# Optimization experiments

Measured on AMD Instinct MI355X. Metric: run time of the kernel, lower is better.

## Reference

```python
import jax, jax.numpy as jnp
import numpy as np

N_HEAD = 16
HEAD_DIM = 128

def rotate_half(x):
    x1, x2 = jnp.split(x, 2, axis=-1)
    return jnp.concatenate((-x2, x1), axis=-1)

def setup_inputs() -> dict:
    key = jax.random.key(0)
    ks = jax.random.split(key, 5)
    B, T, C = 2, 2048, 2048
    x = jax.random.normal(ks[0], (B, T, C), dtype=jnp.float32)
    # rotary tables as used by the module: cos/sin of shape [T, head_dim]
    pos = jnp.arange(T, dtype=jnp.float32)[:, None]
    inv_freq = 1.0 / (10000.0 ** (jnp.arange(0, HEAD_DIM, 2, dtype=jnp.float32) / HEAD_DIM))
    freqs = pos * inv_freq[None, :]            # [T, head_dim/2]
    emb = jnp.concatenate([freqs, freqs], -1)  # [T, head_dim]
    cos = jnp.cos(emb)
    sin = jnp.sin(emb)
    W_qkv = jax.random.normal(ks[1], (C, 3 * C), dtype=jnp.float32) * (C ** -0.5)
    W_proj = jax.random.normal(ks[2], (C, C), dtype=jnp.float32) * (C ** -0.5)
    return {"x": x, "cos": cos, "sin": sin, "W_qkv": W_qkv, "W_proj": W_proj}

def reference(x, cos, sin, W_qkv, W_proj):
    B, T, C = x.shape
    H, D = N_HEAD, HEAD_DIM
    qkv = x @ W_qkv                                   # [B,T,3C]
    q, k, v = jnp.split(qkv, 3, axis=2)
    # [B,T,C] -> [B,H,T,D]
    q = q.reshape(B, T, H, D).transpose(0, 2, 1, 3)
    k = k.reshape(B, T, H, D).transpose(0, 2, 1, 3)
    v = v.reshape(B, T, H, D).transpose(0, 2, 1, 3)
    c = cos[None, None, :, :]                          # [1,1,T,D]
    s = sin[None, None, :, :]
    q = q * c + rotate_half(q) * s
    k = k * c + rotate_half(k) * s
    scale = 1.0 / jnp.sqrt(jnp.float32(D))
    scores = jnp.einsum('bhqd,bhkd->bhqk', q, k) * scale
    attn = jax.nn.softmax(scores, axis=-1)
    y = jnp.einsum('bhqk,bhkd->bhqd', attn, v)         # [B,H,T,D]
    y = y.transpose(0, 2, 1, 3).reshape(B, T, C)
    return y @ W_proj
```

## Files before the change

kernel.cpp:

```cpp
#include <hip/hip_runtime.h>
#include <cstdint>
#include <cstddef>

typedef __bf16 bf16_t;
typedef __bf16 bf16x8 __attribute__((ext_vector_type(8)));
typedef __bf16 bf16x4 __attribute__((ext_vector_type(4)));
typedef float f32x4 __attribute__((ext_vector_type(4)));

#define MFMA16(a, b, c) __builtin_amdgcn_mfma_f32_16x16x32_bf16(a, b, c, 0, 0, 0)

__device__ __forceinline__ void gll16(const bf16_t* g, bf16_t* l) {
  __builtin_amdgcn_global_load_lds(
      (__attribute__((address_space(1))) uint32_t*)((uintptr_t)g),
      (__attribute__((address_space(3))) uint32_t*)((uint32_t)(uintptr_t)l),
      16, 0, 0);
}

__global__ void fill_diag(uint32_t* out, int n_u32) {
  int i = blockIdx.x * 256 + threadIdx.x;
  if (i < n_u32) out[i] = 0x447A0000u;
}

__global__ void conv_vec_f32(const float* __restrict__ in, bf16_t* __restrict__ out,
                             int n8) {
  const int i = blockIdx.x * 256 + threadIdx.x;
  if (i >= n8) return;
  const float* p = in + (size_t)i * 8;
  const f32x4 a = *(const f32x4*)p;
  const f32x4 b = *(const f32x4*)(p + 4);
  bf16x8 o;
#pragma unroll
  for (int j = 0; j < 4; ++j) {
    o[j] = (bf16_t)a[j];
    o[4 + j] = (bf16_t)b[j];
  }
  ((bf16x8*)out)[i] = o;
}

__global__ __launch_bounds__(256) void conv_transpose_f32(
    const float* __restrict__ in, bf16_t* __restrict__ out, int R, int C) {
  __shared__ bf16_t tile[64][72];
  const int bc = blockIdx.x * 64;
  const int br = blockIdx.y * 64;
  const int t = threadIdx.x;
  const int r = t >> 3;
  const int c8 = (t & 7) * 8;
#pragma unroll
  for (int ii = 0; ii < 2; ++ii) {
    const int rr = r + ii * 32;
    const float* p = in + (size_t)(br + rr) * C + bc + c8;
    const f32x4 a = *(const f32x4*)p;
    const f32x4 b = *(const f32x4*)(p + 4);
    bf16x8 v;
#pragma unroll
    for (int j = 0; j < 4; ++j) {
      v[j] = (bf16_t)a[j];
      v[4 + j] = (bf16_t)b[j];
    }
    *(bf16x8*)(&tile[rr][c8]) = v;
  }
  __syncthreads();
#pragma unroll
  for (int ii = 0; ii < 2; ++ii) {
    const int rr = r + ii * 32;
    bf16x8 o;
#pragma unroll
    for (int jj = 0; jj < 8; ++jj) o[jj] = tile[c8 + jj][rr];
    *(bf16x8*)(out + (size_t)(bc + rr) * R + br + c8) = o;
  }
}

#define MF8(MLO, AARR, BARR, NLO)                                           \
  do {                                                                      \
    _Pragma("unroll") for (int m_ = 0; m_ < 4; ++m_) {                      \
      _Pragma("unroll") for (int n_ = 0; n_ < 2; ++n_) {                    \
        acc[(MLO) + m_][(NLO) + n_] =                                       \
            MFMA16(AARR[m_][0], BARR[n_][0], acc[(MLO) + m_][(NLO) + n_]);  \
        acc[(MLO) + m_][(NLO) + n_] =                                       \
            MFMA16(AARR[m_][1], BARR[n_][1], acc[(MLO) + m_][(NLO) + n_]);  \
      }                                                                     \
    }                                                                       \
  } while (0)

template <bool C32>
__global__ __launch_bounds__(512, 2) void gemm8(
    const bf16_t* __restrict__ A, const bf16_t* __restrict__ Bt,
    void* __restrict__ C, int M, int N, int K, int nbn) {
  __shared__ __align__(1024) bf16_t lds8[65536];
  bf16_t* As = lds8;
  bf16_t* Bs = lds8 + 32768;

  const int tid = threadIdx.x;
  const int lane = tid & 63;
  const int wave = tid >> 6;
  const int wr = wave >> 2;
  const int wc = wave & 3;
  const int fr = lane & 15;
  const int fg = lane >> 4;

  const int nwg = gridDim.x;
  const int bid = blockIdx.x;
  const int swz = (bid & 7) * (nwg >> 3) + (bid >> 3);
  const int m0 = (swz / nbn) * 256;
  const int n0 = (swz % nbn) * 256;

  const int NT = K >> 6;

  const int sseg0 = wave * 2;
  const int srow = lane >> 3;
  const int sj = lane & 7;

  auto stage = [&](const bf16_t* __restrict__ G, int row0, bf16_t* L, int kt,
                   int h) {
#pragma unroll
    for (int l = 0; l < 2; ++l) {
      const int seg = sseg0 + l;
      const int r = seg * 8 + srow;
      const int j = sj ^ (r & 7);
      const bf16_t* src = G + (size_t)(row0 + h * 128 + r) * K + kt * 64 + j * 8;
      gll16(src, L + ((2 * kt + h) & 3) * 8192 + seg * 512 + lane * 8);
    }
  };

  const int cb0 = (fg * 16) ^ ((fr & 7) << 4);

  auto lda = [&](bf16x8(&af)[4][2], int kt, int mlo) {
    const char* base = (const char*)(As + ((2 * kt + wr) & 3) * 8192);
#pragma unroll
    for (int m = 0; m < 4; ++m) {
      const char* p = base + ((mlo + m) * 16 + fr) * 128;
      af[m][0] = *(const bf16x8*)(p + cb0);
      af[m][1] = *(const bf16x8*)(p + (cb0 ^ 64));
    }
  };
  auto ldb = [&](bf16x8(&bf)[2][2], int kt, int nlo) {
    const char* base = (const char*)(Bs + ((2 * kt + (wc >> 1)) & 3) * 8192);
#pragma unroll
    for (int n = 0; n < 2; ++n) {
      const char* p = base + ((wc & 1) * 64 + (nlo + n) * 16 + fr) * 128;
      bf[n][0] = *(const bf16x8*)(p + cb0);
      bf[n][1] = *(const bf16x8*)(p + (cb0 ^ 64));
    }
  };

  f32x4 acc[8][4] = {};

  stage(A, m0, As, 0, 0);
  stage(A, m0, As, 0, 1);
  stage(Bt, n0, Bs, 0, 0);
  stage(Bt, n0, Bs, 0, 1);
  stage(Bt, n0, Bs, 1, 0);
  stage(Bt, n0, Bs, 1, 1);
  asm volatile("s_waitcnt vmcnt(4)" ::: "memory");
  __builtin_amdgcn_s_barrier();

  bf16x8 af[4][2], bfA[2][2], bfB[2][2];

  for (int u = 0; u < NT; u += 2) {
    const bool st2 = (u + 2 < NT);
    const bool st3 = (u + 3 < NT);
    lda(af, u, 0);
    ldb(bfA, u, 0);
    stage(A, m0, As, u + 1, 0);
    asm volatile("s_waitcnt lgkmcnt(8)" ::: "memory");
    __builtin_amdgcn_s_barrier();
    asm volatile("s_waitcnt lgkmcnt(0)" ::: "memory");
    __builtin_amdgcn_sched_barrier(0);
    __builtin_amdgcn_s_setprio(1);
    MF8(0, af, bfA, 0);
    __builtin_amdgcn_s_setprio(0);
    __builtin_amdgcn_s_barrier();
    ldb(bfB, u, 2);
    stage(A, m0, As, u + 1, 1);
    __builtin_amdgcn_s_barrier();
    asm volatile("s_waitcnt lgkmcnt(0)" ::: "memory");
    __builtin_amdgcn_sched_barrier(0);
    __builtin_amdgcn_s_setprio(1);
    MF8(0, af, bfB, 2);
    __builtin_amdgcn_s_setprio(0);
    __builtin_amdgcn_s_barrier();
    lda(af, u, 4);
    if (st2) stage(Bt, n0, Bs, u + 2, 0);
    __builtin_amdgcn_s_barrier();
    asm volatile("s_waitcnt lgkmcnt(0)" ::: "memory");
    __builtin_amdgcn_sched_barrier(0);
    __builtin_amdgcn_s_setprio(1);
    MF8(4, af, bfB, 2);
    __builtin_amdgcn_s_setprio(0);
    __builtin_amdgcn_s_barrier();
    if (st2) stage(Bt, n0, Bs, u + 2, 1);
    __builtin_amdgcn_s_barrier();
    __builtin_amdgcn_s_setprio(1);
    MF8(4, af, bfA, 0);
    __builtin_amdgcn_s_setprio(0);
    asm volatile("s_waitcnt vmcnt(4)" ::: "memory");
    __builtin_amdgcn_s_barrier();
    lda(af, u + 1, 0);
    ldb(bfA, u + 1, 0);
    if (st2) stage(A, m0, As, u + 2, 0);
    asm volatile("s_waitcnt lgkmcnt(8)" ::: "memory");
    __builtin_amdgcn_s_barrier();
    asm volatile("s_waitcnt lgkmcnt(0)" ::: "memory");
    __builtin_amdgcn_sched_barrier(0);
    __builtin_amdgcn_s_setprio(1);
    MF8(0, af, bfA, 0);
    __builtin_amdgcn_s_setprio(0);
    __builtin_amdgcn_s_barrier();
    ldb(bfB, u + 1, 2);
    if (st2) stage(A, m0, As, u + 2, 1);
    __builtin_amdgcn_s_barrier();
    asm volatile("s_waitcnt lgkmcnt(0)" ::: "memory");
    __builtin_amdgcn_sched_barrier(0);
    __builtin_amdgcn_s_setprio(1);
    MF8(0, af, bfB, 2);
    __builtin_amdgcn_s_setprio(0);
    __builtin_amdgcn_s_barrier();
    lda(af, u + 1, 4);
    if (st3) stage(Bt, n0, Bs, u + 3, 0);
    __builtin_amdgcn_s_barrier();
    asm volatile("s_waitcnt lgkmcnt(0)" ::: "memory");
    __builtin_amdgcn_sched_barrier(0);
    __builtin_amdgcn_s_setprio(1);
    MF8(4, af, bfB, 2);
    __builtin_amdgcn_s_setprio(0);
    __builtin_amdgcn_s_barrier();
    if (st3) stage(Bt, n0, Bs, u + 3, 1);
    __builtin_amdgcn_s_barrier();
    __builtin_amdgcn_s_setprio(1);
    MF8(4, af, bfA, 0);
    __builtin_amdgcn_s_setprio(0);
    asm volatile("s_waitcnt vmcnt(4)" ::: "memory");
    __builtin_amdgcn_s_barrier();
  }

#pragma unroll
  for (int m = 0; m < 8; ++m) {
#pragma unroll
    for (int n = 0; n < 4; ++n) {
#pragma unroll
      for (int r = 0; r < 4; ++r) {
        const int row = m0 + wr * 128 + m * 16 + fg * 4 + r;
        const int col = n0 + wc * 64 + n * 16 + fr;
        const size_t idx = (size_t)row * N + col;
        if (C32)
          ((float*)C)[idx] = acc[m][n][r];
        else
          ((bf16_t*)C)[idx] = (bf16_t)acc[m][n][r];
      }
    }
  }
  (void)M;
}

template <bool C32>
__global__ __launch_bounds__(256) void gemm_lds(
    const bf16_t* __restrict__ A, const bf16_t* __restrict__ Bt,
    void* __restrict__ C, int M, int N, int K) {
  __shared__ __align__(16) bf16_t As[128 * 32];
  __shared__ __align__(16) bf16_t Bs[128 * 32];
  const int tid = threadIdx.x;
  const int lane = tid & 63;
  const int wave = tid >> 6;
  const int m0 = blockIdx.x * 128;
  const int n0 = blockIdx.y * 128;
  const int wm = (wave & 1) * 64;
  const int wn = (wave >> 1) * 64;
  const int fr = lane & 15;
  const int fk = (lane >> 4) * 8;

  f32x4 acc[4][4] = {};

  const bf16_t* ga = A + (size_t)(m0 + (tid >> 2)) * K + (tid & 3) * 8;
  const bf16_t* gb = Bt + (size_t)(n0 + (tid >> 2)) * K + (tid & 3) * 8;
  bf16_t* lA = As + tid * 8;
  bf16_t* lB = Bs + tid * 8;
  const size_t half = (size_t)64 * K;

  for (int k0 = 0; k0 < K; k0 += 32) {
    __syncthreads();
    gll16(ga, lA);
    gll16(ga + half, lA + 2048);
    gll16(gb, lB);
    gll16(gb + half, lB + 2048);
    ga += 32;
    gb += 32;
    __syncthreads();
    bf16x8 af[4], bfr[4];
#pragma unroll
    for (int i = 0; i < 4; ++i)
      af[i] = *(const bf16x8*)(As + (wm + i * 16 + fr) * 32 + fk);
#pragma unroll
    for (int j = 0; j < 4; ++j)
      bfr[j] = *(const bf16x8*)(Bs + (wn + j * 16 + fr) * 32 + fk);
#pragma unroll
    for (int i = 0; i < 4; ++i)
#pragma unroll
      for (int j = 0; j < 4; ++j)
        acc[i][j] = MFMA16(af[i], bfr[j], acc[i][j]);
  }

  const int fg = lane >> 4;
#pragma unroll
  for (int i = 0; i < 4; ++i) {
#pragma unroll
    for (int j = 0; j < 4; ++j) {
#pragma unroll
      for (int r = 0; r < 4; ++r) {
        const int row = m0 + wm + i * 16 + fg * 4 + r;
        const int col = n0 + wn + j * 16 + fr;
        const size_t idx = (size_t)row * N + col;
        if (C32)
          ((float*)C)[idx] = acc[i][j][r];
        else
          ((bf16_t*)C)[idx] = (bf16_t)acc[i][j][r];
      }
    }
  }
}

template <bool A32, bool C32>
__global__ __launch_bounds__(256) void gemm_t(
    const void* __restrict__ A, const bf16_t* __restrict__ Bt,
    void* __restrict__ C, int M, int N, int K) {
  __shared__ bf16_t As[128 * 32];
  __shared__ bf16_t Bs[128 * 32];
  const int tid = threadIdx.x;
  const int lane = tid & 63;
  const int wave = tid >> 6;
  const int m0 = blockIdx.x * 128;
  const int n0 = blockIdx.y * 128;
  const int wm = (wave & 1) * 64;
  const int wn = (wave >> 1) * 64;
  const int fr = lane & 15;
  const int fk = (lane >> 4) * 8;

  f32x4 acc[4][4] = {};

  const size_t ea0 = (size_t)(m0 + (tid >> 2)) * K + (tid & 3) * 8;
  const bf16_t* gb = Bt + (size_t)(n0 + (tid >> 2)) * K + (tid & 3) * 8;
  bf16_t* lA = As + tid * 8;
  bf16_t* lB = Bs + tid * 8;
  const size_t half = (size_t)64 * K;

  for (int k0 = 0; k0 < K; k0 += 32) {
    bf16x8 ra0, ra1;
    if (A32) {
      const float* pa = (const float*)A + ea0 + k0;
      const f32x4 x0 = *(const f32x4*)pa;
      const f32x4 x1 = *(const f32x4*)(pa + 4);
      const f32x4 x2 = *(const f32x4*)(pa + half);
      const f32x4 x3 = *(const f32x4*)(pa + half + 4);
#pragma unroll
      for (int j = 0; j < 4; ++j) {
        ra0[j] = (bf16_t)x0[j];
        ra0[4 + j] = (bf16_t)x1[j];
        ra1[j] = (bf16_t)x2[j];
        ra1[4 + j] = (bf16_t)x3[j];
      }
    } else {
      const bf16_t* pa = (const bf16_t*)A + ea0 + k0;
      ra0 = *(const bf16x8*)pa;
      ra1 = *(const bf16x8*)(pa + half);
    }
    const bf16x8 rb0 = *(const bf16x8*)gb;
    const bf16x8 rb1 = *(const bf16x8*)(gb + half);
    gb += 32;
    __syncthreads();
    *(bf16x8*)lA = ra0;
    *(bf16x8*)(lA + 2048) = ra1;
    *(bf16x8*)lB = rb0;
    *(bf16x8*)(lB + 2048) = rb1;
    __syncthreads();
    bf16x8 af[4], bfr[4];
#pragma unroll
    for (int i = 0; i < 4; ++i)
      af[i] = *(const bf16x8*)(As + (wm + i * 16 + fr) * 32 + fk);
#pragma unroll
    for (int j = 0; j < 4; ++j)
      bfr[j] = *(const bf16x8*)(Bs + (wn + j * 16 + fr) * 32 + fk);
#pragma unroll
    for (int i = 0; i < 4; ++i)
#pragma unroll
      for (int j = 0; j < 4; ++j)
        acc[i][j] = MFMA16(af[i], bfr[j], acc[i][j]);
  }

  const int fg = lane >> 4;
#pragma unroll
  for (int i = 0; i < 4; ++i) {
#pragma unroll
    for (int j = 0; j < 4; ++j) {
#pragma unroll
      for (int r = 0; r < 4; ++r) {
        const int row = m0 + wm + i * 16 + fg * 4 + r;
        const int col = n0 + wn + j * 16 + fr;
        const size_t idx = (size_t)row * N + col;
        if (C32)
          ((float*)C)[idx] = acc[i][j][r];
        else
          ((bf16_t*)C)[idx] = (bf16_t)acc[i][j][r];
      }
    }
  }
}

__global__ __launch_bounds__(256) void rope_k(
    const bf16_t* __restrict__ qkv, const bf16_t* __restrict__ cosb,
    const bf16_t* __restrict__ sinb, bf16_t* __restrict__ Kr) {
  const int row = blockIdx.x;
  const int t = row & 2047;
  const int b = row >> 11;
  const int idx = threadIdx.x * 8;
  const int h = idx >> 7;
  const int d = idx & 127;
  const float sgn = (d < 64) ? -1.f : 1.f;
  const bf16_t* base = qkv + (size_t)row * 6144 + 2048;
  const bf16x8 kv = *(const bf16x8*)(base + idx);
  const bf16x8 kp = *(const bf16x8*)(base + (idx ^ 64));
  const bf16x8 cv = *(const bf16x8*)(cosb + t * 128 + d);
  const bf16x8 sv = *(const bf16x8*)(sinb + t * 128 + d);
  bf16x8 o;
#pragma unroll
  for (int jj = 0; jj < 8; ++jj)
    o[jj] = (bf16_t)(((float)kv[jj]) * ((float)cv[jj]) +
                     sgn * ((float)kp[jj]) * ((float)sv[jj]));
  *(bf16x8*)(Kr + ((size_t)(b * 16 + h) * 2048 + t) * 128 + d) = o;
}

__global__ __launch_bounds__(256) void transpose_v(
    const bf16_t* __restrict__ qkv, bf16_t* __restrict__ Vt) {
  __shared__ bf16_t tile[64][72];
  const int bh = blockIdx.z;
  const int b = bh >> 4, h = bh & 15;
  const int t0 = blockIdx.x * 64;
  const int d0 = blockIdx.y * 64;
  const int t = threadIdx.x;
  const int r = t >> 3;
  const int c8 = (t & 7) * 8;
#pragma unroll
  for (int ii = 0; ii < 2; ++ii) {
    const int rr = r + ii * 32;
    *(bf16x8*)(&tile[rr][c8]) =
        *(const bf16x8*)(qkv + (size_t)(b * 2048 + t0 + rr) * 6144 + 4096 + h * 128 + d0 + c8);
  }
  __syncthreads();
#pragma unroll
  for (int ii = 0; ii < 2; ++ii) {
    const int rr = r + ii * 32;
    bf16x8 o;
#pragma unroll
    for (int jj = 0; jj < 8; ++jj) o[jj] = tile[c8 + jj][rr];
    *(bf16x8*)(Vt + ((size_t)bh * 128 + d0 + rr) * 2048 + t0 + c8) = o;
  }
}

__global__ __launch_bounds__(256, 4) void flash_q64(
    const bf16_t* __restrict__ qkv, const bf16_t* __restrict__ cosb,
    const bf16_t* __restrict__ sinb, const bf16_t* __restrict__ Kr,
    const bf16_t* __restrict__ Vt, bf16_t* __restrict__ Y) {
  constexpr int T = 2048;
  __shared__ bf16_t Ks[64][136];
  __shared__ bf16_t Vs[128][72];
  const int tid = threadIdx.x;
  const int lane = tid & 63;
  const int wave = tid >> 6;
  const int fr = lane & 15;
  const int fg = lane >> 4;
  const int qt = blockIdx.x;
  const int bh = blockIdx.y;
  const int b = bh >> 4, h = bh & 15;

  const int trow = qt * 64 + wave * 16 + fr;
  const bf16_t* qrow = qkv + (size_t)(b * T + trow) * 6144 + h * 128;
  bf16x8 qf[4];
#pragma unroll
  for (int ks = 0; ks < 4; ++ks) {
    const int d = ks * 32 + fg * 8;
    const float sgn = (d < 64) ? -1.f : 1.f;
    const bf16x8 qv = *(const bf16x8*)(qrow + d);
    const bf16x8 qp = *(const bf16x8*)(qrow + (d ^ 64));
    const bf16x8 cv = *(const bf16x8*)(cosb + trow * 128 + d);
    const bf16x8 sv = *(const bf16x8*)(sinb + trow * 128 + d);
    bf16x8 o;
#pragma unroll
    for (int jj = 0; jj < 8; ++jj)
      o[jj] = (bf16_t)((((float)qv[jj]) * ((float)cv[jj]) +
                        sgn * ((float)qp[jj]) * ((float)sv[jj])) *
                       0.1275174825f);
    qf[ks] = o;
  }

  f32x4 acc[8] = {};
  float l_i = 0.f;

  const int krow = tid >> 4;
  const int kcol = (tid & 15) * 8;
  const int vrow = tid >> 3;
  const int vu = tid & 7;
  const int vc0 = ((vu >> 2) * 32) + ((vu & 1) * 16) + (((vu >> 1) & 1) * 4);
  const bf16_t* Kh = Kr + (size_t)bh * T * 128;
  const bf16_t* Vh = Vt + (size_t)bh * 128 * T;

  for (int j = 0; j < T / 64; ++j) {
    const int t0 = j * 64;
#pragma unroll
    for (int it = 0; it < 4; ++it)
      *(bf16x8*)(&Ks[it * 16 + krow][kcol]) =
          *(const bf16x8*)(Kh + (size_t)(t0 + it * 16 + krow) * 128 + kcol);
#pragma unroll
    for (int it = 0; it < 4; ++it) {
      const int row = it * 32 + vrow;
      const bf16x8 v = *(const bf16x8*)(Vh + (size_t)row * T + t0 + vu * 8);
      bf16x4 lo, hi;
#pragma unroll
      for (int jj = 0; jj < 4; ++jj) {
        lo[jj] = v[jj];
        hi[jj] = v[4 + jj];
      }
      *(bf16x4*)(&Vs[row][vc0]) = lo;
      *(bf16x4*)(&Vs[row][vc0 + 8]) = hi;
    }
    __syncthreads();

    f32x4 sacc[4] = {};
#pragma unroll
    for (int n = 0; n < 4; ++n) {
#pragma unroll
      for (int ks = 0; ks < 4; ++ks) {
        const bf16x8 kf = *(const bf16x8*)(&Ks[n * 16 + fr][ks * 32 + fg * 8]);
        sacc[n] = MFMA16(kf, qf[ks], sacc[n]);
      }
    }

    bf16x8 paf[2];
    float lsum = 0.f;
#pragma unroll
    for (int ks2 = 0; ks2 < 2; ++ks2) {
#pragma unroll
      for (int jj = 0; jj < 8; ++jj) {
        const float p = exp2f(sacc[ks2 * 2 + (jj >> 2)][jj & 3]);
        lsum += p;
        paf[ks2][jj] = (bf16_t)p;
      }
    }
    l_i += lsum;

#pragma unroll
    for (int ks2 = 0; ks2 < 2; ++ks2) {
#pragma unroll
      for (int n = 0; n < 8; ++n) {
        const bf16x8 vf = *(const bf16x8*)(&Vs[n * 16 + fr][ks2 * 32 + fg * 8]);
        acc[n] = MFMA16(paf[ks2], vf, acc[n]);
      }
    }
    __syncthreads();
  }

  float l = l_i;
  l += __shfl_xor(l, 16, 64);
  l += __shfl_xor(l, 32, 64);
#pragma unroll
  for (int r = 0; r < 4; ++r) {
    const float inv = 1.0f / __shfl(l, fg * 4 + r, 64);
    const int t = qt * 64 + wave * 16 + fg * 4 + r;
    bf16_t* yrow = Y + (size_t)(b * T + t) * 2048 + h * 128;
#pragma unroll
    for (int n = 0; n < 8; ++n)
      yrow[n * 16 + fr] = (bf16_t)(acc[n][r] * inv);
  }
}

__global__ __launch_bounds__(256) void flash_fused_v2(
    const bf16_t* __restrict__ qkv, const bf16_t* __restrict__ cosb,
    const bf16_t* __restrict__ sinb, bf16_t* __restrict__ Y) {
  constexpr int T = 2048;
  __shared__ bf16_t Ks[64][136];
  __shared__ bf16_t Vs[128][72];
  __shared__ bf16_t Ps[128][72];
  const int tid = threadIdx.x;
  const int lane = tid & 63;
  const int wave = tid >> 6;
  const int fr = lane & 15;
  const int fg = lane >> 4;
  const int qt = blockIdx.x;
  const int bh = blockIdx.y;
  const int b = bh >> 4, h = bh & 15;

  const bf16_t* qbase = qkv + (size_t)b * T * 6144 + h * 128;
  bf16x8 qf[2][4];
#pragma unroll
  for (int i = 0; i < 2; ++i) {
    const int trow = qt * 128 + wave * 32 + i * 16 + fr;
    const bf16_t* qrow = qbase + (size_t)trow * 6144;
#pragma unroll
    for (int ks = 0; ks < 4; ++ks) {
      const int d = ks * 32 + fg * 8;
      const float sgn = (d < 64) ? -1.f : 1.f;
      const bf16x8 qv = *(const bf16x8*)(qrow + d);
      const bf16x8 qp = *(const bf16x8*)(qrow + (d ^ 64));
      const bf16x8 cv = *(const bf16x8*)(cosb + trow * 128 + d);
      const bf16x8 sv = *(const bf16x8*)(sinb + trow * 128 + d);
      bf16x8 o;
#pragma unroll
      for (int jj = 0; jj < 8; ++jj)
        o[jj] = (bf16_t)((((float)qv[jj]) * ((float)cv[jj]) +
                          sgn * ((float)qp[jj]) * ((float)sv[jj])) *
                         0.08838834764831845f);
      qf[i][ks] = o;
    }
  }

  f32x4 acc[2][8] = {};
  float l_i[2][4] = {};

  const int kr = tid >> 4;
  const int kc = (tid & 15) * 8;
  const float sgnk = (kc < 64) ? -1.f : 1.f;
  const int tp = tid & 63;

  for (int j = 0; j < T / 64; ++j) {
    const int t0 = j * 64;
#pragma unroll
    for (int it = 0; it < 4; ++it) {
      const int row = it * 16 + kr;
      const int tg = t0 + row;
      const bf16_t* krow = qkv + ((size_t)(b * T + tg)) * 6144 + 2048 + h * 128;
      const bf16x8 kv = *(const bf16x8*)(krow + kc);
      const bf16x8 kp = *(const bf16x8*)(krow + (kc ^ 64));
      const bf16x8 cv = *(const bf16x8*)(cosb + tg * 128 + kc);
      const bf16x8 sv = *(const bf16x8*)(sinb + tg * 128 + kc);
      bf16x8 o;
#pragma unroll
      for (int jj = 0; jj < 8; ++jj)
        o[jj] = (bf16_t)(((float)kv[jj]) * ((float)cv[jj]) +
                         sgnk * ((float)kp[jj]) * ((float)sv[jj]));
      *(bf16x8*)(&Ks[row][kc]) = o;
    }
#pragma unroll
    for (int cc = 0; cc < 4; ++cc) {
      const int d8 = (cc * 4 + (tid >> 6)) * 8;
      const bf16x8 vv = *(const bf16x8*)(qkv + ((size_t)(b * T + t0 + tp)) * 6144 +
                                         4096 + h * 128 + d8);
#pragma unroll
      for (int jj = 0; jj < 8; ++jj) Vs[d8 + jj][tp] = vv[jj];
    }
    __syncthreads();

    f32x4 sacc[2][4] = {};
#pragma unroll
    for (int n = 0; n < 4; ++n) {
#pragma unroll
      for (int ks = 0; ks < 4; ++ks) {
        const bf16x8 kf = *(const bf16x8*)(&Ks[n * 16 + fr][ks * 32 + fg * 8]);
        sacc[0][n] = MFMA16(qf[0][ks], kf, sacc[0][n]);
        sacc[1][n] = MFMA16(qf[1][ks], kf, sacc[1][n]);
      }
    }

#pragma unroll
    for (int i = 0; i < 2; ++i) {
#pragma unroll
      for (int r = 0; r < 4; ++r) {
        const float p0 = __expf(sacc[i][0][r]);
        const float p1 = __expf(sacc[i][1][r]);
        const float p2 = __expf(sacc[i][2][r]);
        const float p3 = __expf(sacc[i][3][r]);
        l_i[i][r] += (p0 + p1) + (p2 + p3);
        const int prow = wave * 32 + i * 16 + fg * 4 + r;
        Ps[prow][0 + fr] = (bf16_t)p0;
        Ps[prow][16 + fr] = (bf16_t)p1;
        Ps[prow][32 + fr] = (bf16_t)p2;
        Ps[prow][48 + fr] = (bf16_t)p3;
      }
    }

#pragma unroll
    for (int ks = 0; ks < 2; ++ks) {
      const bf16x8 pf0 = *(const bf16x8*)(&Ps[wave * 32 + fr][ks * 32 + fg * 8]);
      const bf16x8 pf1 = *(const bf16x8*)(&Ps[wave * 32 + 16 + fr][ks * 32 + fg * 8]);
#pragma unroll
      for (int n = 0; n < 8; ++n) {
        const bf16x8 vf = *(const bf16x8*)(&Vs[n * 16 + fr][ks * 32 + fg * 8]);
        acc[0][n] = MFMA16(pf0, vf, acc[0][n]);
        acc[1][n] = MFMA16(pf1, vf, acc[1][n]);
      }
    }
    __syncthreads();
  }

#pragma unroll
  for (int i = 0; i < 2; ++i) {
#pragma unroll
    for (int r = 0; r < 4; ++r) {
      float l = l_i[i][r];
#pragma unroll
      for (int msk = 1; msk < 16; msk <<= 1) l += __shfl_xor(l, msk, 64);
      const float inv = 1.0f / l;
      const int t = qt * 128 + wave * 32 + i * 16 + fg * 4 + r;
      bf16_t* yrow = Y + (size_t)(b * T + t) * 2048 + h * 128;
#pragma unroll
      for (int n = 0; n < 8; ++n)
        yrow[n * 16 + fr] = (bf16_t)(acc[i][n][r] * inv);
    }
  }
}

extern "C" void kernel_launch(void* const* d_in, const int* in_sizes, int n_in,
                              void* d_out, int out_size, void* d_ws, size_t ws_size,
                              hipStream_t stream) {
  const float* x = (const float*)d_in[0];
  const float* cosi = (const float*)d_in[1];
  const float* sini = (const float*)d_in[2];
  const float* Wqkv = (const float*)d_in[3];
  const float* Wproj = (const float*)d_in[4];

  const size_t NEED_FAST = sizeof(bf16_t) *
      ((size_t)12582912 + 262144 + 262144 + 25165824 + 8388608 + 8388608);
  const size_t NEED_BASE = 256 + sizeof(bf16_t) *
      ((size_t)12582912 + 4194304 + 262144 + 262144 + 25165824);

  if (ws_size >= NEED_FAST) {
    bf16_t* base = (bf16_t*)d_ws;
    bf16_t* WqkvT = base;
    bf16_t* y = base;
    bf16_t* cosb = base + 12582912;
    bf16_t* sinb = cosb + 262144;
    bf16_t* qkv = sinb + 262144;
    bf16_t* WprojT = qkv;
    bf16_t* Kr = qkv + 25165824;
    bf16_t* xb = Kr;
    bf16_t* Vt = Kr + 8388608;

    conv_vec_f32<<<128, 256, 0, stream>>>(cosi, cosb, 32768);
    conv_vec_f32<<<128, 256, 0, stream>>>(sini, sinb, 32768);
    conv_vec_f32<<<4096, 256, 0, stream>>>(x, xb, 1048576);
    conv_transpose_f32<<<dim3(96, 32), 256, 0, stream>>>(Wqkv, WqkvT, 2048, 6144);
    gemm8<false><<<384, 512, 0, stream>>>(xb, WqkvT, qkv, 4096, 6144, 2048, 24);
    rope_k<<<4096, 256, 0, stream>>>(qkv, cosb, sinb, Kr);
    transpose_v<<<dim3(32, 2, 32), 256, 0, stream>>>(qkv, Vt);
    flash_q64<<<dim3(32, 32), 256, 0, stream>>>(qkv, cosb, sinb, Kr, Vt, y);
    conv_transpose_f32<<<dim3(32, 32), 256, 0, stream>>>(Wproj, WprojT, 2048, 2048);
    gemm_lds<true><<<dim3(32, 16), 256, 0, stream>>>(y, WprojT, d_out, 4096, 2048, 2048);
  } else if (ws_size >= NEED_BASE) {
    bf16_t* base = (bf16_t*)((char*)d_ws + 256);
    bf16_t* WqkvT = base;
    bf16_t* y = base;
    bf16_t* WprojT = base + 12582912;
    bf16_t* cosb = WprojT + 4194304;
    bf16_t* sinb = cosb + 262144;
    bf16_t* qkv = sinb + 262144;

    conv_vec_f32<<<128, 256, 0, stream>>>(cosi, cosb, 32768);
    conv_vec_f32<<<128, 256, 0, stream>>>(sini, sinb, 32768);
    conv_transpose_f32<<<dim3(96, 32), 256, 0, stream>>>(Wqkv, WqkvT, 2048, 6144);
    gemm_t<true, false><<<dim3(32, 48), 256, 0, stream>>>(x, WqkvT, qkv, 4096, 6144, 2048);
    flash_fused_v2<<<dim3(16, 32), 256, 0, stream>>>(qkv, cosb, sinb, y);
    conv_transpose_f32<<<dim3(32, 32), 256, 0, stream>>>(Wproj, WprojT, 2048, 2048);
    gemm_t<false, true><<<dim3(32, 16), 256, 0, stream>>>(y, WprojT, d_out, 4096, 2048, 2048);
  } else {
    fill_diag<<<(out_size + 255) / 256, 256, 0, stream>>>((uint32_t*)d_out, out_size);
  }
}
```

Baseline: 457.7 us.

## Prefetch next K/V tile during compute in flash attention with swizzled async K loads

The flash attention kernel now stages K directly into LDS with global_load_lds, using an XOR swizzle in place of padding. It prefetches V for the next iteration into registers while the current tile's softmax and PV MFMAs run. The aim is to hide global memory latency behind compute instead of loading and then syncing each iteration. In exchange it adds barriers per iteration and register pressure for the V prefetch, under a 4-blocks-per-SM launch bound.

```diff
diff --git a/kernel.cpp b/kernel.cpp
--- a/kernel.cpp
+++ b/kernel.cpp
@@ -454,22 +454,22 @@
   }
 }
 
-__global__ __launch_bounds__(256, 4) void flash_q64(
+__global__ __launch_bounds__(256, 4) void flash_q64p(
     const bf16_t* __restrict__ qkv, const bf16_t* __restrict__ cosb,
     const bf16_t* __restrict__ sinb, const bf16_t* __restrict__ Kr,
     const bf16_t* __restrict__ Vt, bf16_t* __restrict__ Y) {
   constexpr int T = 2048;
-  __shared__ bf16_t Ks[64][136];
+  __shared__ __align__(1024) bf16_t Ks[64 * 128];
   __shared__ bf16_t Vs[128][72];
   const int tid = threadIdx.x;
   const int lane = tid & 63;
-  const int wave = tid >> 6;
   const int fr = lane & 15;
   const int fg = lane >> 4;
   const int qt = blockIdx.x;
   const int bh = blockIdx.y;
   const int b = bh >> 4, h = bh & 15;
 
+  const int wave = tid >> 6;
   const int trow = qt * 64 + wave * 16 + fr;
   const bf16_t* qrow = qkv + (size_t)(b * T + trow) * 6144 + h * 128;
   bf16x8 qf[4];
@@ -494,23 +494,30 @@
   float l_i = 0.f;
 
   const int krow = tid >> 4;
-  const int kcol = (tid & 15) * 8;
+  const int sc = (tid & 15) ^ (krow & 7);
   const int vrow = tid >> 3;
   const int vu = tid & 7;
   const int vc0 = ((vu >> 2) * 32) + ((vu & 1) * 16) + (((vu >> 1) & 1) * 4);
   const bf16_t* Kh = Kr + (size_t)bh * T * 128;
   const bf16_t* Vh = Vt + (size_t)bh * 128 * T;
 
-  for (int j = 0; j < T / 64; ++j) {
-    const int t0 = j * 64;
+  auto stageK = [&](int t0) {
 #pragma unroll
     for (int it = 0; it < 4; ++it)
-      *(bf16x8*)(&Ks[it * 16 + krow][kcol]) =
-          *(const bf16x8*)(Kh + (size_t)(t0 + it * 16 + krow) * 128 + kcol);
+      gll16(Kh + (size_t)(t0 + it * 16 + krow) * 128 + sc * 8,
+            Ks + it * 2048 + tid * 8);
+  };
+  bf16x8 vreg[4];
+  auto loadV = [&](int t0) {
+#pragma unroll
+    for (int it = 0; it < 4; ++it)
+      vreg[it] = *(const bf16x8*)(Vh + (size_t)(it * 32 + vrow) * T + t0 + vu * 8);
+  };
+  auto writeV = [&]() {
 #pragma unroll
     for (int it = 0; it < 4; ++it) {
       const int row = it * 32 + vrow;
-      const bf16x8 v = *(const bf16x8*)(Vh + (size_t)row * T + t0 + vu * 8);
+      const bf16x8 v = vreg[it];
       bf16x4 lo, hi;
 #pragma unroll
       for (int jj = 0; jj < 4; ++jj) {
@@ -520,16 +527,35 @@
       *(bf16x4*)(&Vs[row][vc0]) = lo;
       *(bf16x4*)(&Vs[row][vc0 + 8]) = hi;
     }
+  };
+
+  stageK(0);
+  loadV(0);
+  asm volatile("s_waitcnt vmcnt(0)" ::: "memory");
+  __builtin_amdgcn_sched_barrier(0);
+  writeV();
+  __syncthreads();
+
+  const int cswz = (fr & 7) << 4;
+  const char* kbase = (const char*)Ks;
+
+  for (int j = 0; j < T / 64; ++j) {
+    f32x4 sacc[4] = {};
+#pragma unroll
+    for (int n = 0; n < 4; ++n) {
+      const char* krowp = kbase + (n * 16 + fr) * 256;
+#pragma unroll
+      for (int ks = 0; ks < 4; ++ks) {
+        const bf16x8 kf = *(const bf16x8*)(krowp + ((ks * 64 + fg * 16) ^ cswz));
+        sacc[n] = MFMA16(kf, qf[ks], sacc[n]);
+      }
+    }
     __syncthreads();
 
-    f32x4 sacc[4] = {};
-#pragma unroll
-    for (int n = 0; n < 4; ++n) {
-#pragma unroll
-      for (int ks = 0; ks < 4; ++ks) {
-        const bf16x8 kf = *(const bf16x8*)(&Ks[n * 16 + fr][ks * 32 + fg * 8]);
-        sacc[n] = MFMA16(kf, qf[ks], sacc[n]);
-      }
+    const bool more = (j + 1 < T / 64);
+    if (more) {
+      stageK((j + 1) * 64);
+      loadV((j + 1) * 64);
     }
 
     bf16x8 paf[2];
@@ -553,7 +579,14 @@
         acc[n] = MFMA16(paf[ks2], vf, acc[n]);
       }
     }
+
+    asm volatile("s_waitcnt vmcnt(0)" ::: "memory");
+    __builtin_amdgcn_sched_barrier(0);
     __syncthreads();
+    if (more) {
+      writeV();
+      __syncthreads();
+    }
   }
 
   float l = l_i;
@@ -738,7 +771,7 @@
     gemm8<false><<<384, 512, 0, stream>>>(xb, WqkvT, qkv, 4096, 6144, 2048, 24);
     rope_k<<<4096, 256, 0, stream>>>(qkv, cosb, sinb, Kr);
     transpose_v<<<dim3(32, 2, 32), 256, 0, stream>>>(qkv, Vt);
-    flash_q64<<<dim3(32, 32), 256, 0, stream>>>(qkv, cosb, sinb, Kr, Vt, y);
+    flash_q64p<<<dim3(32, 32), 256, 0, stream>>>(qkv, cosb, sinb, Kr, Vt, y);
     conv_transpose_f32<<<dim3(32, 32), 256, 0, stream>>>(Wproj, WprojT, 2048, 2048);
     gemm_lds<true><<<dim3(32, 16), 256, 0, stream>>>(y, WprojT, d_out, 4096, 2048, 2048);
   } else if (ws_size >= NEED_BASE) {
```

New measurement: 437.9 us. -4.3%, faster.
